# Kernel tuning notes

Measured on AMD Instinct MI355X. Metric: run time of the kernel, lower is better.

## Reference

```python
import jax, jax.numpy as jnp
import numpy as np

N, E, H, C, IN = 50000, 500000, 4, 64, 256


def setup_inputs() -> dict:
    key = jax.random.key(0)
    ks = jax.random.split(key, 16)
    sW = 1.0 / np.sqrt(IN)
    sA = 1.0 / np.sqrt(C)
    inp = {
        "x": jax.random.normal(ks[0], (N, IN), jnp.float32),
        "edge_index": jax.random.randint(ks[1], (2, E), 0, N, jnp.int64 if jax.config.jax_enable_x64 else jnp.int32),
        "W1": jax.random.normal(ks[2], (IN, H * C), jnp.float32) * sW,
        "as1": jax.random.normal(ks[3], (H, C), jnp.float32) * sA,
        "ad1": jax.random.normal(ks[4], (H, C), jnp.float32) * sA,
        "b1": jnp.zeros((H * C,), jnp.float32),
        "W2": jax.random.normal(ks[5], (H * C, H * C), jnp.float32) * sW,
        "as2": jax.random.normal(ks[6], (H, C), jnp.float32) * sA,
        "ad2": jax.random.normal(ks[7], (H, C), jnp.float32) * sA,
        "b2": jnp.zeros((H * C,), jnp.float32),
        "WN": jax.random.normal(ks[8], (H * C, H * C), jnp.float32) * sW,
        "asN": jax.random.normal(ks[9], (H, C), jnp.float32) * sA,
        "adN": jax.random.normal(ks[10], (H, C), jnp.float32) * sA,
        "bN": jnp.zeros((H * C,), jnp.float32),
    }
    return inp


def _gat_conv(x, src, dst, W, a_src, a_dst, b, n_nodes):
    # x: [N, F_in]; src/dst: [E'] (self-loops included); W: [F_in, H*C]
    Hh, Cc = a_src.shape
    h = (x @ W).reshape(n_nodes, Hh, Cc)                      # [N,H,C]
    e_src = jnp.einsum("nhc,hc->nh", h, a_src)                # [N,H]
    e_dst = jnp.einsum("nhc,hc->nh", h, a_dst)
    e = jax.nn.leaky_relu(e_src[src] + e_dst[dst], 0.2)       # [E',H]
    m = jax.lax.stop_gradient(jax.ops.segment_max(e, dst, num_segments=n_nodes))
    ex = jnp.exp(e - m[dst])
    denom = jax.ops.segment_sum(ex, dst, num_segments=n_nodes)
    alpha = ex / (denom[dst] + 1e-16)                         # [E',H]
    out = jax.ops.segment_sum(h[src] * alpha[:, :, None], dst, num_segments=n_nodes)
    return out.reshape(n_nodes, Hh * Cc) + b


def reference(x, edge_index, W1, as1, ad1, b1, W2, as2, ad2, b2, WN, asN, adN, bN):
    n = x.shape[0]
    loops = jnp.arange(n, dtype=edge_index.dtype)
    src = jnp.concatenate([edge_index[0], loops])  # PyG GATConv add_self_loops=True
    dst = jnp.concatenate([edge_index[1], loops])
    inp = x
    h = jax.nn.relu(_gat_conv(x, src, dst, W1, as1, ad1, b1, n)) + inp
    h = jax.nn.relu(_gat_conv(h, src, dst, W2, as2, ad2, b2, n))
    h = _gat_conv(h, src, dst, WN, asN, adN, bN, n)
    # eval mode: F.dropout is identity
    return jax.nn.relu(h + inp)
```

## Files before the change

kernel.cpp:

```cpp
#include <hip/hip_runtime.h>
#include <hip/hip_bf16.h>
#include <math.h>

typedef short short8 __attribute__((ext_vector_type(8)));
typedef float f32x4 __attribute__((ext_vector_type(4)));

static __device__ __forceinline__ float bfu(unsigned short u) {
    union { unsigned int i; float f; } c; c.i = ((unsigned int)u) << 16; return c.f;
}
static __device__ __forceinline__ ushort f2bu(float f) {
    __hip_bfloat16 h = __float2bfloat16(f);
    return *(ushort*)&h;
}
static __device__ __forceinline__ void gload_lds16(const void* g, void* l) {
    __builtin_amdgcn_global_load_lds(
        (const __attribute__((address_space(1))) void*)g,
        (__attribute__((address_space(3))) void*)l, 16, 0, 0);
}


__global__ __launch_bounds__(256) void k_wt_cast3(const float* __restrict__ W1, const float* __restrict__ W2,
                           const float* __restrict__ W3, __hip_bfloat16* __restrict__ Wt1,
                           __hip_bfloat16* __restrict__ Wt2, __hip_bfloat16* __restrict__ Wt3) {
    __shared__ float t[64][65];
    const float* W = (blockIdx.z == 0) ? W1 : (blockIdx.z == 1) ? W2 : W3;
    __hip_bfloat16* Wt = (blockIdx.z == 0) ? Wt1 : (blockIdx.z == 1) ? Wt2 : Wt3;
    int k0 = blockIdx.x * 64, n0 = blockIdx.y * 64;
#pragma unroll
    for (int i = 0; i < 16; ++i) {
        int idx = threadIdx.x + 256 * i;
        int r = idx >> 6, c = idx & 63;
        t[r][c] = W[(size_t)(k0 + r) * 256 + n0 + c];
    }
    __syncthreads();
#pragma unroll
    for (int i = 0; i < 16; ++i) {
        int idx = threadIdx.x + 256 * i;
        int r = idx >> 6, c = idx & 63;
        Wt[(size_t)(n0 + r) * 256 + k0 + c] = __float2bfloat16(t[c][r]);
    }
}


__global__ void k_hist(const int* __restrict__ dstv, int* __restrict__ cnt, int E, int Nn) {
    int i = blockIdx.x * blockDim.x + threadIdx.x;
    if (i < E) atomicAdd(&cnt[dstv[i]], 1);
    else if (i < E + Nn) atomicAdd(&cnt[i - E], 1);
}

__global__ void k_scan1(const int* __restrict__ cnt, int* __restrict__ excl, int* __restrict__ bsum, int n) {
    __shared__ int s[256];
    int i = blockIdx.x * 256 + threadIdx.x;
    int v = (i < n) ? cnt[i] : 0;
    s[threadIdx.x] = v;
    __syncthreads();
    for (int off = 1; off < 256; off <<= 1) {
        int t = (threadIdx.x >= off) ? s[threadIdx.x - off] : 0;
        __syncthreads();
        s[threadIdx.x] += t;
        __syncthreads();
    }
    if (i < n) excl[i] = s[threadIdx.x] - v;
    if (threadIdx.x == 255) bsum[blockIdx.x] = s[255];
}

__global__ void k_scan2(const int* __restrict__ bsum, int* __restrict__ boff, int nb) {
    __shared__ int s[256];
    int carry = 0;
    for (int base = 0; base < nb; base += 256) {
        int i = base + threadIdx.x;
        int v = (i < nb) ? bsum[i] : 0;
        s[threadIdx.x] = v;
        __syncthreads();
        for (int off = 1; off < 256; off <<= 1) {
            int t = (threadIdx.x >= off) ? s[threadIdx.x - off] : 0;
            __syncthreads();
            s[threadIdx.x] += t;
            __syncthreads();
        }
        if (i < nb) boff[i] = carry + s[threadIdx.x] - v;
        carry += s[255];
        __syncthreads();
    }
}

__global__ void k_scan3(const int* __restrict__ excl, const int* __restrict__ boff,
                        int* __restrict__ rowptr, int* __restrict__ cursor, int n, int Etot) {
    int i = blockIdx.x * blockDim.x + threadIdx.x;
    if (i < n) {
        int v = excl[i] + boff[i >> 8];
        rowptr[i] = v;
        cursor[i] = v;
    }
    if (i == 0) rowptr[n] = Etot;
}

__global__ void k_scatter(const int* __restrict__ srcv, const int* __restrict__ dstv,
                          int* __restrict__ cursor, int* __restrict__ colsrc, int E, int Nn) {
    int i = blockIdx.x * blockDim.x + threadIdx.x;
    if (i < E) {
        int pos = atomicAdd(&cursor[dstv[i]], 1);
        colsrc[pos] = srcv[i];
    } else if (i < E + Nn) {
        int nn = i - E;
        int pos = atomicAdd(&cursor[nn], 1);
        colsrc[pos] = nn;
    }
}


template <bool AFP32>
__global__ __launch_bounds__(256) void k_gemm(const void* __restrict__ Ap,
                                              const __hip_bfloat16* __restrict__ Wt,
                                              __hip_bfloat16* __restrict__ C,
                                              const float* __restrict__ a_src,
                                              const float* __restrict__ a_dst,
                                              float* __restrict__ es,
                                              float* __restrict__ ed, int M) {
    __shared__ __align__(16) char As[64 * 128];
    __shared__ __align__(16) char Bs[256 * 128];
    int tid = threadIdx.x;
    int w = tid >> 6, l = tid & 63;
    int lo = l & 15, hi = l >> 4;
    int m0 = blockIdx.x * 64;
    f32x4 acc[4][4];
#pragma unroll
    for (int a = 0; a < 4; ++a)
#pragma unroll
        for (int b = 0; b < 4; ++b) acc[a][b] = (f32x4){0.f, 0.f, 0.f, 0.f};

    for (int bk = 0; bk < 256; bk += 64) {
        __syncthreads();
        if (AFP32) {
#pragma unroll
            for (int i = 0; i < 2; ++i) {
                int c = tid + 256 * i;
                int row = c >> 3, ko = c & 7;
                int rg = m0 + row;
                uint4 v = {0u, 0u, 0u, 0u};
                if (rg < M) {
                    const float* Af = (const float*)Ap;
                    float4 f0 = *(const float4*)(Af + (size_t)rg * 256 + bk + ko * 8);
                    float4 f1 = *(const float4*)(Af + (size_t)rg * 256 + bk + ko * 8 + 4);
                    v.x = (uint)f2bu(f0.x) | ((uint)f2bu(f0.y) << 16);
                    v.y = (uint)f2bu(f0.z) | ((uint)f2bu(f0.w) << 16);
                    v.z = (uint)f2bu(f1.x) | ((uint)f2bu(f1.y) << 16);
                    v.w = (uint)f2bu(f1.z) | ((uint)f2bu(f1.w) << 16);
                }
                *(uint4*)(As + row * 128 + ((ko * 16) ^ ((row & 7) << 4))) = v;
            }
        } else {
#pragma unroll
            for (int i = 0; i < 2; ++i) {
                int c = tid + 256 * i;
                int row = c >> 3, ko = c & 7;
                gload_lds16((const char*)Ap + (size_t)(m0 + row) * 512 + bk * 2 +
                                ((ko * 16) ^ ((row & 7) << 4)),
                            As + (i * 256 + w * 64) * 16);
            }
        }
#pragma unroll
        for (int i = 0; i < 8; ++i) {
            int c = tid + 256 * i;
            int row = c >> 3, ko = c & 7;
            gload_lds16((const char*)Wt + (size_t)row * 512 + bk * 2 +
                            ((ko * 16) ^ ((row & 7) << 4)),
                        Bs + (i * 256 + w * 64) * 16);
        }
        __syncthreads();
#pragma unroll
        for (int kk = 0; kk < 2; ++kk) {
            int koff = kk * 64 + hi * 16;
            short8 af[4], bfr[4];
#pragma unroll
            for (int mi = 0; mi < 4; ++mi) {
                int row = mi * 16 + lo;
                af[mi] = *(const short8*)(As + row * 128 + (koff ^ ((row & 7) << 4)));
            }
#pragma unroll
            for (int ni = 0; ni < 4; ++ni) {
                int row = w * 64 + ni * 16 + lo;
                bfr[ni] = *(const short8*)(Bs + row * 128 + (koff ^ ((row & 7) << 4)));
            }
#pragma unroll
            for (int mi = 0; mi < 4; ++mi)
#pragma unroll
                for (int ni = 0; ni < 4; ++ni)
                    acc[mi][ni] = __builtin_amdgcn_mfma_f32_16x16x32_bf16(af[mi], bfr[ni], acc[mi][ni], 0, 0, 0);
        }
    }
#pragma unroll
    for (int mi = 0; mi < 4; ++mi) {
#pragma unroll
        for (int r = 0; r < 4; ++r) {
            int rg = m0 + mi * 16 + hi * 4 + r;
            if (rg < M) {
#pragma unroll
                for (int ni = 0; ni < 4; ++ni) {
                    int col = w * 64 + ni * 16 + lo;
                    C[(size_t)rg * 256 + col] = __float2bfloat16(acc[mi][ni][r]);
                }
            }
        }
    }
    float avv[4], adv[4];
#pragma unroll
    for (int ni = 0; ni < 4; ++ni) {
        avv[ni] = a_src[w * 64 + ni * 16 + lo];
        adv[ni] = a_dst[w * 64 + ni * 16 + lo];
    }
#pragma unroll
    for (int mi = 0; mi < 4; ++mi) {
#pragma unroll
        for (int r = 0; r < 4; ++r) {
            int rg = m0 + mi * 16 + hi * 4 + r;
            float s1 = 0.f, s2 = 0.f;
#pragma unroll
            for (int ni = 0; ni < 4; ++ni) {
                s1 += acc[mi][ni][r] * avv[ni];
                s2 += acc[mi][ni][r] * adv[ni];
            }
#pragma unroll
            for (int mk = 1; mk < 16; mk <<= 1) {
                s1 += __shfl_xor(s1, mk, 64);
                s2 += __shfl_xor(s2, mk, 64);
            }
            if (lo == 0 && rg < M) {
                es[rg * 4 + w] = s1;
                ed[rg * 4 + w] = s2;
            }
        }
    }
}


__global__ __launch_bounds__(256) void k_aggregate(const __hip_bfloat16* __restrict__ hW,
                            const int* __restrict__ rowptr,
                            const int* __restrict__ colsrc, const float* __restrict__ es,
                            const float* __restrict__ edv_, const float* __restrict__ bias,
                            const float* __restrict__ xres, __hip_bfloat16* __restrict__ outbf,
                            float* __restrict__ outf, int mode, int Nn) {
    int n = blockIdx.x * 4 + (threadIdx.x >> 6);
    if (n >= Nn) return;
    int l = threadIdx.x & 63;
    int h = l >> 4;
    int r0 = rowptr[n];
    int deg = rowptr[n + 1] - r0;
    float edv = edv_[n * 4 + h];

    float denom = 0.f;
    float a0 = 0.f, a1 = 0.f, a2 = 0.f, a3 = 0.f;
    const ushort* hw = (const ushort*)hW;
    int sfb = colsrc[r0];

    for (int base = 0; base < deg; base += 8) {
        int sv[8];
#pragma unroll
        for (int u = 0; u < 8; ++u)
            sv[u] = (base + u < deg) ? colsrc[r0 + base + u] : sfb;
        float ev[8];
#pragma unroll
        for (int u = 0; u < 8; ++u)
            ev[u] = es[(size_t)sv[u] * 4 + h];
        uint2 hv[8];
#pragma unroll
        for (int u = 0; u < 8; ++u)
            hv[u] = *(const uint2*)(hw + (size_t)sv[u] * 256 + l * 4);
#pragma unroll
        for (int u = 0; u < 8; ++u) {
            float t = ev[u] + edv;
            t = fmaxf(t, 0.2f * t);
            float p = (base + u < deg) ? __expf(t) : 0.f;
            denom += p;
            a0 += p * bfu((ushort)(hv[u].x & 0xffff));
            a1 += p * bfu((ushort)(hv[u].x >> 16));
            a2 += p * bfu((ushort)(hv[u].y & 0xffff));
            a3 += p * bfu((ushort)(hv[u].y >> 16));
        }
    }

    float inv = 1.f / (denom + 1e-16f);
    int idx = n * 256 + l * 4;
    float4 b4 = *(const float4*)(bias + l * 4);
    float v0 = a0 * inv + b4.x;
    float v1 = a1 * inv + b4.y;
    float v2 = a2 * inv + b4.z;
    float v3 = a3 * inv + b4.w;

    if (mode == 2) {
        float4 x4 = *(const float4*)(xres + idx);
        float4 o;
        o.x = fmaxf(v0 + x4.x, 0.f);
        o.y = fmaxf(v1 + x4.y, 0.f);
        o.z = fmaxf(v2 + x4.z, 0.f);
        o.w = fmaxf(v3 + x4.w, 0.f);
        *(float4*)(outf + idx) = o;
    } else {
        v0 = fmaxf(v0, 0.f); v1 = fmaxf(v1, 0.f);
        v2 = fmaxf(v2, 0.f); v3 = fmaxf(v3, 0.f);
        if (mode == 0) {
            float4 x4 = *(const float4*)(xres + idx);
            v0 += x4.x; v1 += x4.y; v2 += x4.z; v3 += x4.w;
        }
        union { ushort u[4]; uint2 v; } o;
        o.u[0] = f2bu(v0); o.u[1] = f2bu(v1);
        o.u[2] = f2bu(v2); o.u[3] = f2bu(v3);
        *(uint2*)((ushort*)outbf + idx) = o.v;
    }
}


extern "C" void kernel_launch(void* const* d_in, const int* in_sizes, int n_in,
                              void* d_out, int out_size, void* d_ws, size_t ws_size,
                              hipStream_t stream) {
    const float* x  = (const float*)d_in[0];
    const int* ei   = (const int*)d_in[1];
    const float* W1 = (const float*)d_in[2];
    const float* as1 = (const float*)d_in[3];
    const float* ad1 = (const float*)d_in[4];
    const float* b1  = (const float*)d_in[5];
    const float* W2  = (const float*)d_in[6];
    const float* as2 = (const float*)d_in[7];
    const float* ad2 = (const float*)d_in[8];
    const float* b2  = (const float*)d_in[9];
    const float* WN  = (const float*)d_in[10];
    const float* asN = (const float*)d_in[11];
    const float* adN = (const float*)d_in[12];
    const float* bN  = (const float*)d_in[13];

    int Nn = in_sizes[0] / 256;
    int E = in_sizes[1] / 2;
    const int* srcv = ei;
    const int* dstv = ei + E;
    int Etot = E + Nn;

    char* p = (char*)d_ws;
    auto alloc = [&](size_t bytes) {
        char* r = p;
        p += (bytes + 255) & ~(size_t)255;
        return r;
    };
    __hip_bfloat16* Pbf  = (__hip_bfloat16*)alloc((size_t)Nn * 256 * 2 + 32768);
    __hip_bfloat16* Qbf  = (__hip_bfloat16*)alloc((size_t)Nn * 256 * 2 + 32768);
    __hip_bfloat16* hWbf = (__hip_bfloat16*)alloc((size_t)Nn * 256 * 2);
    __hip_bfloat16* Wt1  = (__hip_bfloat16*)alloc(256 * 256 * 2);
    __hip_bfloat16* Wt2  = (__hip_bfloat16*)alloc(256 * 256 * 2);
    __hip_bfloat16* Wt3  = (__hip_bfloat16*)alloc(256 * 256 * 2);
    float* esrc = (float*)alloc((size_t)Nn * 4 * 4);
    float* edst = (float*)alloc((size_t)Nn * 4 * 4);
    int* cnt    = (int*)alloc((size_t)Nn * 4);
    int* excl   = (int*)alloc((size_t)Nn * 4);
    int* rowptr = (int*)alloc((size_t)(Nn + 1) * 4);
    int* cursor = (int*)alloc((size_t)Nn * 4);
    int* bsum   = (int*)alloc(4096);
    int* boff   = (int*)alloc(4096);
    int* colsrc = (int*)alloc((size_t)Etot * 4);

    int nb = (Nn + 255) / 256;

    dim3 wg(4, 4, 3);
    k_wt_cast3<<<wg, 256, 0, stream>>>(W1, W2, WN, Wt1, Wt2, Wt3);

    hipMemsetAsync(cnt, 0, (size_t)Nn * 4, stream);
    k_hist<<<(Etot + 255) / 256, 256, 0, stream>>>(dstv, cnt, E, Nn);
    k_scan1<<<nb, 256, 0, stream>>>(cnt, excl, bsum, Nn);
    k_scan2<<<1, 256, 0, stream>>>(bsum, boff, nb);
    k_scan3<<<nb, 256, 0, stream>>>(excl, boff, rowptr, cursor, Nn, Etot);
    k_scatter<<<(Etot + 255) / 256, 256, 0, stream>>>(srcv, dstv, cursor, colsrc, E, Nn);

    int gg = (Nn + 63) / 64;
    int ga = (Nn + 3) / 4;

    k_gemm<true><<<gg, 256, 0, stream>>>(x, Wt1, hWbf, as1, ad1, esrc, edst, Nn);
    k_aggregate<<<ga, 256, 0, stream>>>(hWbf, rowptr, colsrc, esrc, edst, b1, x, Pbf, nullptr, 0, Nn);
    k_gemm<false><<<gg, 256, 0, stream>>>(Pbf, Wt2, hWbf, as2, ad2, esrc, edst, Nn);
    k_aggregate<<<ga, 256, 0, stream>>>(hWbf, rowptr, colsrc, esrc, edst, b2, x, Qbf, nullptr, 1, Nn);
    k_gemm<false><<<gg, 256, 0, stream>>>(Qbf, Wt3, hWbf, asN, adN, esrc, edst, Nn);
    k_aggregate<<<ga, 256, 0, stream>>>(hWbf, rowptr, colsrc, esrc, edst, bN, x, nullptr, (float*)d_out, 2, Nn);
}
```

Before: 295.5 us.

## Double-buffer edge gathers in aggregate and fold count memset into weight cast

The aggregation loop is software-pipelined with two register buffers, so the next 8 neighbour indices, scores and feature rows are loaded while the current batch is accumulated. This hides gather latency behind arithmetic, at the cost of roughly doubling the loop's register use, which may lower occupancy. Separately, zeroing the histogram counts moves from a hipMemsetAsync call into the weight-transpose kernel, removing one launch.

```diff
diff --git a/kernel.cpp b/kernel.cpp
--- a/kernel.cpp
+++ b/kernel.cpp
@@ -21,7 +21,8 @@
 
 __global__ __launch_bounds__(256) void k_wt_cast3(const float* __restrict__ W1, const float* __restrict__ W2,
                            const float* __restrict__ W3, __hip_bfloat16* __restrict__ Wt1,
-                           __hip_bfloat16* __restrict__ Wt2, __hip_bfloat16* __restrict__ Wt3) {
+                           __hip_bfloat16* __restrict__ Wt2, __hip_bfloat16* __restrict__ Wt3,
+                           int* __restrict__ cnt, int Nn) {
     __shared__ float t[64][65];
     const float* W = (blockIdx.z == 0) ? W1 : (blockIdx.z == 1) ? W2 : W3;
     __hip_bfloat16* Wt = (blockIdx.z == 0) ? Wt1 : (blockIdx.z == 1) ? Wt2 : Wt3;
@@ -39,6 +40,8 @@
         int r = idx >> 6, c = idx & 63;
         Wt[(size_t)(n0 + r) * 256 + k0 + c] = __float2bfloat16(t[c][r]);
     }
+    int bid = blockIdx.x + (blockIdx.y << 2) + (blockIdx.z << 4);
+    for (int i = bid * 256 + threadIdx.x; i < Nn; i += 48 * 256) cnt[i] = 0;
 }
 
 
@@ -234,6 +237,34 @@
 }
 
 
+#define AGG_LOAD(BASE, SV, EV, HV)                                          \
+    {                                                                       \
+        _Pragma("unroll")                                                   \
+        for (int u = 0; u < 8; ++u)                                         \
+            SV[u] = ((BASE) + u < deg) ? colsrc[r0 + (BASE) + u] : sfb;     \
+        _Pragma("unroll")                                                   \
+        for (int u = 0; u < 8; ++u)                                         \
+            EV[u] = es[(size_t)SV[u] * 4 + h];                              \
+        _Pragma("unroll")                                                   \
+        for (int u = 0; u < 8; ++u)                                         \
+            HV[u] = *(const uint2*)(hw + (size_t)SV[u] * 256 + l * 4);      \
+    }
+
+#define AGG_CONS(BASE, EV, HV)                                              \
+    {                                                                       \
+        _Pragma("unroll")                                                   \
+        for (int u = 0; u < 8; ++u) {                                       \
+            float t = EV[u] + edv;                                          \
+            t = fmaxf(t, 0.2f * t);                                         \
+            float p = ((BASE) + u < deg) ? __expf(t) : 0.f;                 \
+            denom += p;                                                     \
+            a0 += p * bfu((ushort)(HV[u].x & 0xffff));                      \
+            a1 += p * bfu((ushort)(HV[u].x >> 16));                         \
+            a2 += p * bfu((ushort)(HV[u].y & 0xffff));                      \
+            a3 += p * bfu((ushort)(HV[u].y >> 16));                         \
+        }                                                                   \
+    }
+
 __global__ __launch_bounds__(256) void k_aggregate(const __hip_bfloat16* __restrict__ hW,
                             const int* __restrict__ rowptr,
                             const int* __restrict__ colsrc, const float* __restrict__ es,
@@ -253,30 +284,22 @@
     const ushort* hw = (const ushort*)hW;
     int sfb = colsrc[r0];
 
-    for (int base = 0; base < deg; base += 8) {
-        int sv[8];
-#pragma unroll
-        for (int u = 0; u < 8; ++u)
-            sv[u] = (base + u < deg) ? colsrc[r0 + base + u] : sfb;
-        float ev[8];
-#pragma unroll
-        for (int u = 0; u < 8; ++u)
-            ev[u] = es[(size_t)sv[u] * 4 + h];
-        uint2 hv[8];
-#pragma unroll
-        for (int u = 0; u < 8; ++u)
-            hv[u] = *(const uint2*)(hw + (size_t)sv[u] * 256 + l * 4);
-#pragma unroll
-        for (int u = 0; u < 8; ++u) {
-            float t = ev[u] + edv;
-            t = fmaxf(t, 0.2f * t);
-            float p = (base + u < deg) ? __expf(t) : 0.f;
-            denom += p;
-            a0 += p * bfu((ushort)(hv[u].x & 0xffff));
-            a1 += p * bfu((ushort)(hv[u].x >> 16));
-            a2 += p * bfu((ushort)(hv[u].y & 0xffff));
-            a3 += p * bfu((ushort)(hv[u].y >> 16));
-        }
+    int sA[8]; float eA[8]; uint2 hA[8];
+    int sB[8]; float eB[8]; uint2 hB[8];
+
+    int base = 0;
+    AGG_LOAD(0, sA, eA, hA);
+    while (true) {
+        int nxt = base + 8;
+        if (nxt < deg) AGG_LOAD(nxt, sB, eB, hB);
+        AGG_CONS(base, eA, hA);
+        base = nxt;
+        if (base >= deg) break;
+        nxt = base + 8;
+        if (nxt < deg) AGG_LOAD(nxt, sA, eA, hA);
+        AGG_CONS(base, eB, hB);
+        base = nxt;
+        if (base >= deg) break;
     }
 
     float inv = 1.f / (denom + 1e-16f);
@@ -359,9 +382,8 @@
     int nb = (Nn + 255) / 256;
 
     dim3 wg(4, 4, 3);
-    k_wt_cast3<<<wg, 256, 0, stream>>>(W1, W2, WN, Wt1, Wt2, Wt3);
-
-    hipMemsetAsync(cnt, 0, (size_t)Nn * 4, stream);
+    k_wt_cast3<<<wg, 256, 0, stream>>>(W1, W2, WN, Wt1, Wt2, Wt3, cnt, Nn);
+
     k_hist<<<(Etot + 255) / 256, 256, 0, stream>>>(dstv, cnt, E, Nn);
     k_scan1<<<nb, 256, 0, stream>>>(cnt, excl, bsum, Nn);
     k_scan2<<<1, 256, 0, stream>>>(bsum, boff, nb);
```

Measured after the change: 319.1 us. 1.08x slower.

## Fuse three-pass scan into single-pass chained scan and fold memset into cast kernel

Applied to the files above, without the earlier changes.

Replaces the three-kernel exclusive scan (block scan, single-block scan of block sums, add-back) with one kernel that chains block prefixes through a flag array in a decoupled, serial-lookback fashion. The zeroing of the histogram counts and the flags is moved into the weight-transpose kernel, removing the memset launch. This cuts kernel launches and intermediate buffers. The chained lookback relies on blocks being scheduled in order, which risks a spin-wait hang if a later block occupies resources while an earlier one is not resident; with 196 blocks that is unlikely to matter.

```diff
diff --git a/kernel.cpp b/kernel.cpp
--- a/kernel.cpp
+++ b/kernel.cpp
@@ -21,7 +21,8 @@
 
 __global__ __launch_bounds__(256) void k_wt_cast3(const float* __restrict__ W1, const float* __restrict__ W2,
                            const float* __restrict__ W3, __hip_bfloat16* __restrict__ Wt1,
-                           __hip_bfloat16* __restrict__ Wt2, __hip_bfloat16* __restrict__ Wt3) {
+                           __hip_bfloat16* __restrict__ Wt2, __hip_bfloat16* __restrict__ Wt3,
+                           int* __restrict__ cnt, int* __restrict__ flags, int Nn, int nb) {
     __shared__ float t[64][65];
     const float* W = (blockIdx.z == 0) ? W1 : (blockIdx.z == 1) ? W2 : W3;
     __hip_bfloat16* Wt = (blockIdx.z == 0) ? Wt1 : (blockIdx.z == 1) ? Wt2 : Wt3;
@@ -39,6 +40,9 @@
         int r = idx >> 6, c = idx & 63;
         Wt[(size_t)(n0 + r) * 256 + k0 + c] = __float2bfloat16(t[c][r]);
     }
+    int bid = blockIdx.x + (blockIdx.y << 2) + (blockIdx.z << 4);
+    for (int i = bid * 256 + threadIdx.x; i < Nn; i += 48 * 256) cnt[i] = 0;
+    if (bid == 0 && threadIdx.x < nb) flags[threadIdx.x] = 0;
 }
 
 
@@ -48,9 +52,14 @@
     else if (i < E + Nn) atomicAdd(&cnt[i - E], 1);
 }
 
-__global__ void k_scan1(const int* __restrict__ cnt, int* __restrict__ excl, int* __restrict__ bsum, int n) {
+__global__ __launch_bounds__(256) void k_scanall(const int* __restrict__ cnt,
+                        int* __restrict__ rowptr, int* __restrict__ cursor,
+                        int* __restrict__ bsum, int* __restrict__ flags,
+                        int n, int Etot) {
     __shared__ int s[256];
-    int i = blockIdx.x * 256 + threadIdx.x;
+    __shared__ int prevs;
+    int b = blockIdx.x;
+    int i = b * 256 + threadIdx.x;
     int v = (i < n) ? cnt[i] : 0;
     s[threadIdx.x] = v;
     __syncthreads();
@@ -60,37 +69,23 @@
         s[threadIdx.x] += t;
         __syncthreads();
     }
-    if (i < n) excl[i] = s[threadIdx.x] - v;
-    if (threadIdx.x == 255) bsum[blockIdx.x] = s[255];
-}
-
-__global__ void k_scan2(const int* __restrict__ bsum, int* __restrict__ boff, int nb) {
-    __shared__ int s[256];
-    int carry = 0;
-    for (int base = 0; base < nb; base += 256) {
-        int i = base + threadIdx.x;
-        int v = (i < nb) ? bsum[i] : 0;
-        s[threadIdx.x] = v;
-        __syncthreads();
-        for (int off = 1; off < 256; off <<= 1) {
-            int t = (threadIdx.x >= off) ? s[threadIdx.x - off] : 0;
-            __syncthreads();
-            s[threadIdx.x] += t;
-            __syncthreads();
-        }
-        if (i < nb) boff[i] = carry + s[threadIdx.x] - v;
-        carry += s[255];
-        __syncthreads();
-    }
-}
-
-__global__ void k_scan3(const int* __restrict__ excl, const int* __restrict__ boff,
-                        int* __restrict__ rowptr, int* __restrict__ cursor, int n, int Etot) {
-    int i = blockIdx.x * blockDim.x + threadIdx.x;
+    if (threadIdx.x == 0) {
+        int p = 0;
+        if (b > 0) {
+            while (atomicAdd(&flags[b - 1], 0) == 0) { }
+            p = bsum[b - 1];
+        }
+        prevs = p;
+        bsum[b] = p + s[255];
+        __threadfence();
+        atomicExch(&flags[b], 1);
+    }
+    __syncthreads();
+    int pr = prevs;
     if (i < n) {
-        int v = excl[i] + boff[i >> 8];
-        rowptr[i] = v;
-        cursor[i] = v;
+        int r = pr + s[threadIdx.x] - v;
+        rowptr[i] = r;
+        cursor[i] = r;
     }
     if (i == 0) rowptr[n] = Etot;
 }
@@ -349,23 +344,19 @@
     float* esrc = (float*)alloc((size_t)Nn * 4 * 4);
     float* edst = (float*)alloc((size_t)Nn * 4 * 4);
     int* cnt    = (int*)alloc((size_t)Nn * 4);
-    int* excl   = (int*)alloc((size_t)Nn * 4);
     int* rowptr = (int*)alloc((size_t)(Nn + 1) * 4);
     int* cursor = (int*)alloc((size_t)Nn * 4);
     int* bsum   = (int*)alloc(4096);
-    int* boff   = (int*)alloc(4096);
+    int* flags  = (int*)alloc(4096);
     int* colsrc = (int*)alloc((size_t)Etot * 4);
 
     int nb = (Nn + 255) / 256;
 
     dim3 wg(4, 4, 3);
-    k_wt_cast3<<<wg, 256, 0, stream>>>(W1, W2, WN, Wt1, Wt2, Wt3);
-
-    hipMemsetAsync(cnt, 0, (size_t)Nn * 4, stream);
+    k_wt_cast3<<<wg, 256, 0, stream>>>(W1, W2, WN, Wt1, Wt2, Wt3, cnt, flags, Nn, nb);
+
     k_hist<<<(Etot + 255) / 256, 256, 0, stream>>>(dstv, cnt, E, Nn);
-    k_scan1<<<nb, 256, 0, stream>>>(cnt, excl, bsum, Nn);
-    k_scan2<<<1, 256, 0, stream>>>(bsum, boff, nb);
-    k_scan3<<<nb, 256, 0, stream>>>(excl, boff, rowptr, cursor, Nn, Etot);
+    k_scanall<<<nb, 256, 0, stream>>>(cnt, rowptr, cursor, bsum, flags, Nn, Etot);
     k_scatter<<<(Etot + 255) / 256, 256, 0, stream>>>(srcv, dstv, cursor, colsrc, E, Nn);
 
     int gg = (Nn + 63) / 64;
```

Measured after the change: 521.4 us. +76.5%, slower.
